# Kernel tuning notes

Measured on AMD Instinct MI355X. Metric: run time of the kernel, lower is better.

Reference implementation:

```python
import jax, jax.numpy as jnp
import numpy as np

B, SST, SL = 16, 256, 48
VOCAB, D, CH = 16384, 64, 112
TPI = 0.0


def setup_inputs() -> dict:
    key = jax.random.key(0)
    ks = jax.random.split(key, 26)
    def n(k, shp, s=0.05):
        return jax.random.normal(k, shp, dtype=jnp.float32) * s
    return {
        "x": jax.random.randint(ks[0], (B, SST), 0, VOCAB),
        "ees": n(ks[1], (B, D, SL), 1.0),
        "emb": n(ks[2], (VOCAB, D)),
        "cl0_w": n(ks[3], (CH, D, 1)),  "cl0_b": n(ks[4], (CH,)),
        "cl1_w": n(ks[5], (CH, CH, 3)), "cl1_b": n(ks[6], (CH,)),
        "claa_w": n(ks[7], (CH, CH, 3)), "claa_b": n(ks[8], (CH,)),
        "clfa_w": n(ks[9], (CH, CH, 3)), "clfa_b": n(ks[10], (CH,)),
        "ccac_w": n(ks[11], (CH, CH, 3)), "ccac_b": n(ks[12], (CH,)),
        "cib_w": n(ks[13], (D, CH, 1)),  "cib_b": n(ks[14], (D,)),
        "cpr1_w": n(ks[15], (D, 2 * D, 1)), "cpr1_b": n(ks[16], (D,)),
        "cpr2_w": n(ks[17], (D, D, 1)),  "cpr2_b": n(ks[18], (D,)),
        "cma_w": n(ks[19], (CH, D, 1)),  "cma_b": n(ks[20], (CH,)),
        "ccf_w": n(ks[21], (D, CH, 1)),  "ccf_b": n(ks[22], (D,)),
        "fff_b": n(ks[23], (VOCAB,)),
    }


def _conv1x1(x, w, b):
    # x: [B,C,S], w: [O,C,1] -> [B,O,S]
    return jnp.einsum('oc,bcs->bos', w[:, :, 0], x) + b[None, :, None]


def _conv3(x, w, b):
    # valid 1D conv, channels-first. x: [B,C,S+2] -> [B,O,S]
    y = jax.lax.conv_general_dilated(x, w, (1,), 'VALID',
                                     dimension_numbers=('NCH', 'OIH', 'NCH'))
    return y + b[None, :, None]


def _forward(x, ees, emb, cl0_w, cl0_b, cl1_w, cl1_b, claa_w, claa_b,
             clfa_w, clfa_b, ccac_w, ccac_b, cib_w, cib_b,
             cpr1_w, cpr1_b, cpr2_w, cpr2_b, cma_w, cma_b,
             ccf_w, ccf_b, fff_b):
    b = x.shape[0]
    pre_d = jnp.transpose(emb[x], (0, 2, 1))            # [B,64,SST]
    t = _conv1x1(pre_d, cl0_w, cl0_b)                   # [B,112,SST]
    tp = jnp.full((b, CH, 2), TPI, dtype=t.dtype)       # tpi pad columns

    # split cpr layer1 weight into the t-half and ees-half (concat along ch)
    wt, we = cpr1_w[:, :D, 0], cpr1_w[:, D:, 0]

    def stage(t_in, conv_w, conv_b):
        tt = jnp.concatenate([tp, t_in], axis=2)        # [B,112,SST+2]
        xconv = jax.nn.relu(_conv3(tt, conv_w, conv_b))  # [B,112,SST]
        c = _conv1x1(xconv, cib_w, cib_b)               # [B,64,SST]
        # all-pairs broadcast (sl x sst) + 1x1-conv MLP, equivalent to
        # repeat/concat/cpr in the original, without duplicating data
        h = (jnp.einsum('oc,bcs->bos', wt, c)[:, :, None, :]
             + jnp.einsum('oc,bcl->bol', we, ees)[:, :, :, None]
             + cpr1_b[None, :, None, None])             # [B,64,SL,SST]
        h = jax.nn.relu(h)
        h = jax.nn.relu(jnp.einsum('oc,bcls->bols', cpr2_w[:, :, 0], h)
                        + cpr2_b[None, :, None, None])
        m = jnp.max(h, axis=2)                          # max over sl -> [B,64,SST]
        return _conv1x1(m, cma_w, cma_b) + xconv        # residual add

    t = stage(t, cl1_w, cl1_b)
    t = stage(t, claa_w, claa_b)
    t = stage(t, clfa_w, clfa_b)
    t = stage(t, ccac_w, ccac_b)

    ccf_out = _conv1x1(t, ccf_w, ccf_b)                 # [B,64,SST]
    # tied-weight output projection: [B,SST,64] @ emb.T -> [B,SST,VOCAB]
    output = jnp.einsum('bds,vd->bsv', ccf_out, emb) + fff_b
    return output, pre_d, ccf_out


def reference(x, ees, emb, cl0_w, cl0_b, cl1_w, cl1_b, claa_w, claa_b,
              clfa_w, clfa_b, ccac_w, ccac_b, cib_w, cib_b,
              cpr1_w, cpr1_b, cpr2_w, cpr2_b, cma_w, cma_b,
              ccf_w, ccf_b, fff_b):
    return _forward(x, ees, emb, cl0_w, cl0_b, cl1_w, cl1_b, claa_w, claa_b,
                    clfa_w, clfa_b, ccac_w, ccac_b, cib_w, cib_b,
                    cpr1_w, cpr1_b, cpr2_w, cpr2_b, cma_w, cma_b,
                    ccf_w, ccf_b, fff_b)
```

## Files before the change

### kernel.cpp

```cpp
#include <hip/hip_runtime.h>

#define B_ 16
#define SST 256
#define SL 48
#define VOCAB 16384
#define D_ 64
#define CH 112

#define OUT0_ELEMS ((size_t)B_*SST*VOCAB)
#define OUT1_ELEMS (B_*D_*SST)

typedef __attribute__((ext_vector_type(8))) short s8v;
typedef __attribute__((ext_vector_type(4))) float f32x4;

#define MFMA(a,b,c) __builtin_amdgcn_mfma_f32_16x16x32_bf16(a, b, c, 0, 0, 0)

__device__ __forceinline__ void split1(float f, unsigned short* h, unsigned short* l) {
    unsigned u = __float_as_uint(f);
    *h = (unsigned short)(u >> 16);
    float lo = f - __uint_as_float(u & 0xffff0000u);
    *l = (unsigned short)(__float_as_uint(lo) >> 16);
}
__device__ __forceinline__ uint2 split_pack2(float f0, float f1) {
    unsigned u0 = __float_as_uint(f0), u1 = __float_as_uint(f1);
    unsigned hp = (u0 >> 16) | (u1 & 0xffff0000u);
    float l0 = f0 - __uint_as_float(u0 & 0xffff0000u);
    float l1 = f1 - __uint_as_float(u1 & 0xffff0000u);
    unsigned lp = (__float_as_uint(l0) >> 16) | (__float_as_uint(l1) & 0xffff0000u);
    return make_uint2(hp, lp);
}

__global__ void e_kernel(const float* __restrict__ ees,
                         const float* __restrict__ cpr1_w,
                         const float* __restrict__ cpr1_b,
                         const float* __restrict__ cib_b,
                         float* __restrict__ Eb) {
    int bl = blockIdx.x;
    int b = bl / SL, l = bl % SL;
    int tid = threadIdx.x;
    __shared__ float ec[D_];
    ec[tid] = ees[(b*D_ + tid)*SL + l];
    __syncthreads();
    const float* wrow = cpr1_w + tid*(2*D_);
    float acc = cpr1_b[tid];
    #pragma unroll
    for (int k = 0; k < D_; ++k) acc += wrow[k]*cib_b[k];
    #pragma unroll
    for (int c = 0; c < D_; ++c) acc += wrow[D_ + c]*ec[c];
    Eb[(b*SL + l)*D_ + tid] = acc;
}

__global__ void emb2bf_kernel(const float* __restrict__ emb,
                              unsigned short* __restrict__ hi,
                              unsigned short* __restrict__ lo) {
    int i = blockIdx.x*256 + threadIdx.x;
    float4 v = reinterpret_cast<const float4*>(emb)[i];
    ushort4 h, l;
    split1(v.x, &h.x, &l.x);
    split1(v.y, &h.y, &l.y);
    split1(v.z, &h.z, &l.z);
    split1(v.w, &h.w, &l.w);
    reinterpret_cast<ushort4*>(hi)[i] = h;
    reinterpret_cast<ushort4*>(lo)[i] = l;
}

__global__ void conv_prep_kernel(const float* __restrict__ w0, const float* __restrict__ w1,
                                 const float* __restrict__ w2, const float* __restrict__ w3,
                                 unsigned short* __restrict__ Wch, unsigned short* __restrict__ Wcl) {
    int gid = blockIdx.x*256 + threadIdx.x;
    int c = gid & 127;
    int o = (gid >> 7) & 127;
    int kst = gid >> 14;
    int k = kst % 3, st = kst / 3;
    const float* w = (st == 0) ? w0 : (st == 1) ? w1 : (st == 2) ? w2 : w3;
    float v = (o < CH && c < CH) ? w[o*CH*3 + c*3 + k] : 0.f;
    unsigned short h, l; split1(v, &h, &l);
    Wch[gid] = h; Wcl[gid] = l;
}

__global__ void shared_prep_kernel(const float* __restrict__ cpr1_w,
                                   const float* __restrict__ cib_w,
                                   const float* __restrict__ cpr2_w,
                                   const float* __restrict__ cma_w,
                                   const float* __restrict__ ccf_w,
                                   const float* __restrict__ cl0_w,
                                   unsigned short* __restrict__ Wcomb_h, unsigned short* __restrict__ Wcomb_l,
                                   unsigned short* __restrict__ W2h, unsigned short* __restrict__ W2l,
                                   unsigned short* __restrict__ cmah, unsigned short* __restrict__ cmal,
                                   unsigned short* __restrict__ ccfh, unsigned short* __restrict__ ccfl,
                                   unsigned short* __restrict__ cl0h, unsigned short* __restrict__ cl0l) {
    int gid = blockIdx.x*256 + threadIdx.x;
    unsigned short h, l;
    if (gid < 8192) {
        int o = gid >> 7, c = gid & 127;
        float v = 0.f;
        if (c < CH) {
            const float* wrow = cpr1_w + o*(2*D_);
            #pragma unroll
            for (int k = 0; k < D_; ++k) v += wrow[k]*cib_w[k*CH + c];
        }
        split1(v, &h, &l); Wcomb_h[gid] = h; Wcomb_l[gid] = l;
    } else if (gid < 12288) {
        int idx = gid - 8192;
        split1(cpr2_w[idx], &h, &l); W2h[idx] = h; W2l[idx] = l;
    } else if (gid < 20480) {
        int idx = gid - 12288;
        int o = idx >> 6;
        float v = (o < CH) ? cma_w[idx] : 0.f;
        split1(v, &h, &l); cmah[idx] = h; cmal[idx] = l;
    } else if (gid < 28672) {
        int idx = gid - 20480;
        int d = idx >> 7, c = idx & 127;
        float v = (c < CH) ? ccf_w[d*CH + c] : 0.f;
        split1(v, &h, &l); ccfh[idx] = h; ccfl[idx] = l;
    } else {
        int idx = gid - 28672;
        int o = idx >> 6;
        float v = (o < CH) ? cl0_w[idx] : 0.f;
        split1(v, &h, &l); cl0h[idx] = h; cl0l[idx] = l;
    }
}

__device__ __forceinline__ void h2max_wave(
    const float* __restrict__ AcRow,
    const float* __restrict__ El,
    const unsigned short* __restrict__ W2h, const unsigned short* __restrict__ W2l,
    int n, int kg, int o_lane, float b2_lane,
    unsigned short* __restrict__ Mmh, unsigned short* __restrict__ Mml, int bs) {
    float4 a00 = *reinterpret_cast<const float4*>(AcRow + kg*8);
    float4 a01 = *reinterpret_cast<const float4*>(AcRow + kg*8 + 4);
    float4 a10 = *reinterpret_cast<const float4*>(AcRow + 32 + kg*8);
    float4 a11 = *reinterpret_cast<const float4*>(AcRow + 32 + kg*8 + 4);

    f32x4 acc[4][3];
    #pragma unroll
    for (int mt = 0; mt < 4; ++mt)
        #pragma unroll
        for (int lt = 0; lt < 3; ++lt)
            acc[mt][lt] = (f32x4){0.f, 0.f, 0.f, 0.f};

    #pragma unroll
    for (int kt = 0; kt < 2; ++kt) {
        int cc = kt*32 + kg*8;
        float4 aA = (kt == 0) ? a00 : a10;
        float4 aB = (kt == 0) ? a01 : a11;
        s8v a2h[4], a2l[4];
        #pragma unroll
        for (int mt = 0; mt < 4; ++mt) {
            a2h[mt] = *(const s8v*)&W2h[(mt*16 + n)*64 + cc];
            a2l[mt] = *(const s8v*)&W2l[(mt*16 + n)*64 + cc];
        }
        #pragma unroll
        for (int lt = 0; lt < 3; ++lt) {
            const float* ep = &El[(lt*16 + n)*68 + cc];
            float4 e0 = *reinterpret_cast<const float4*>(ep);
            float4 e1 = *reinterpret_cast<const float4*>(ep + 4);
            float h0 = fmaxf(aA.x + e0.x, 0.f);
            float h1 = fmaxf(aA.y + e0.y, 0.f);
            float h2 = fmaxf(aA.z + e0.z, 0.f);
            float h3 = fmaxf(aA.w + e0.w, 0.f);
            float h4 = fmaxf(aB.x + e1.x, 0.f);
            float h5 = fmaxf(aB.y + e1.y, 0.f);
            float h6 = fmaxf(aB.z + e1.z, 0.f);
            float h7 = fmaxf(aB.w + e1.w, 0.f);
            uint2 q0 = split_pack2(h0, h1);
            uint2 q1 = split_pack2(h2, h3);
            uint2 q2 = split_pack2(h4, h5);
            uint2 q3 = split_pack2(h6, h7);
            union { unsigned u[4]; s8v v; } Bh, Bl;
            Bh.u[0] = q0.x; Bh.u[1] = q1.x; Bh.u[2] = q2.x; Bh.u[3] = q3.x;
            Bl.u[0] = q0.y; Bl.u[1] = q1.y; Bl.u[2] = q2.y; Bl.u[3] = q3.y;
            #pragma unroll
            for (int mt = 0; mt < 4; ++mt) {
                acc[mt][lt] = MFMA(a2h[mt], Bh.v, acc[mt][lt]);
                acc[mt][lt] = MFMA(a2h[mt], Bl.v, acc[mt][lt]);
                acc[mt][lt] = MFMA(a2l[mt], Bh.v, acc[mt][lt]);
            }
        }
    }

    float mx[16];
    #pragma unroll
    for (int mt = 0; mt < 4; ++mt)
        #pragma unroll
        for (int r = 0; r < 4; ++r)
            mx[mt*4 + r] = fmaxf(fmaxf(acc[mt][0][r], acc[mt][1][r]), acc[mt][2][r]);
    #pragma unroll
    for (int step = 0; step < 4; ++step) {
        int msk = 1 << step;
        #pragma unroll
        for (int i = 0; i < 16; ++i)
            mx[i] = fmaxf(mx[i], __shfl_xor(mx[i], msk));
    }
    float sel = mx[0];
    #pragma unroll
    for (int i = 1; i < 16; ++i)
        sel = (n == i) ? mx[i] : sel;
    float mval = fmaxf(sel + b2_lane, 0.f);
    unsigned short mh, ml; split1(mval, &mh, &ml);
    Mmh[bs*64 + o_lane] = mh;
    Mml[bs*64 + o_lane] = ml;
}

__global__ __launch_bounds__(512) void stage1_kernel(
    const int* __restrict__ x, const float* __restrict__ emb,
    const unsigned short* __restrict__ cl0h, const unsigned short* __restrict__ cl0l,
    const float* __restrict__ cl0_b,
    const unsigned short* __restrict__ Wch, const unsigned short* __restrict__ Wcl,
    const float* __restrict__ conv_b,
    const unsigned short* __restrict__ Wcombh, const unsigned short* __restrict__ Wcombl,
    const float* __restrict__ Eb,
    const unsigned short* __restrict__ W2h, const unsigned short* __restrict__ W2l,
    const float* __restrict__ cpr2_b,
    float* __restrict__ pre_d, float* __restrict__ xc_g,
    unsigned short* __restrict__ Mmh, unsigned short* __restrict__ Mml) {
    int b = blockIdx.x >> 4, s0 = (blockIdx.x & 15) << 4;
    int tid = threadIdx.x, w = tid >> 6, lane = tid & 63, n = lane & 15, kg = lane >> 4;

    __shared__ unsigned short Eg_h[18*72], Eg_l[18*72];
    __shared__ unsigned short Tt_h[18*136], Tt_l[18*136];
    __shared__ unsigned short Xt_h[16*136], Xt_l[16*136];
    __shared__ float El[48*68];
    __shared__ float AcT[16*68];

    for (int idx = tid; idx < 288; idx += 512) {
        int si = idx >> 4, c4 = (idx & 15)*4;
        int s = s0 - 2 + si;
        float4 v = make_float4(0.f, 0.f, 0.f, 0.f);
        if (s >= 0) {
            int tok = x[b*SST + s];
            v = *reinterpret_cast<const float4*>(&emb[tok*D_ + c4]);
        }
        ushort4 h, l;
        split1(v.x, &h.x, &l.x); split1(v.y, &h.y, &l.y);
        split1(v.z, &h.z, &l.z); split1(v.w, &h.w, &l.w);
        *reinterpret_cast<ushort4*>(&Eg_h[si*72 + c4]) = h;
        *reinterpret_cast<ushort4*>(&Eg_l[si*72 + c4]) = l;
        if (si >= 2) {
            pre_d[(b*D_ + c4+0)*SST + s] = v.x;
            pre_d[(b*D_ + c4+1)*SST + s] = v.y;
            pre_d[(b*D_ + c4+2)*SST + s] = v.z;
            pre_d[(b*D_ + c4+3)*SST + s] = v.w;
        }
    }
    for (int idx = tid; idx < 768; idx += 512) {
        int l = idx >> 4, c4 = (idx & 15)*4;
        *reinterpret_cast<float4*>(&El[l*68 + c4]) =
            *reinterpret_cast<const float4*>(&Eb[(b*SL + l)*64 + c4]);
    }
    __syncthreads();

    int ob = w*16 + kg*4;
    #pragma unroll
    for (int ct = 0; ct < 2; ++ct) {
        int si = ct*2 + n;
        f32x4 tv = {0.f, 0.f, 0.f, 0.f};
        #pragma unroll
        for (int kt = 0; kt < 2; ++kt) {
            int cc = kt*32 + kg*8;
            s8v bh = *(const s8v*)&Eg_h[si*72 + cc];
            s8v bl = *(const s8v*)&Eg_l[si*72 + cc];
            int ai = (w*16 + n)*64 + cc;
            s8v ah = *(const s8v*)&cl0h[ai];
            s8v al = *(const s8v*)&cl0l[ai];
            tv = MFMA(ah, bh, tv); tv = MFMA(ah, bl, tv); tv = MFMA(al, bh, tv);
        }
        int s = s0 - 2 + si;
        float r0 = 0.f, r1 = 0.f, r2 = 0.f, r3 = 0.f;
        if (s >= 0) {
            r0 = tv[0] + ((ob+0 < CH) ? cl0_b[ob+0] : 0.f);
            r1 = tv[1] + ((ob+1 < CH) ? cl0_b[ob+1] : 0.f);
            r2 = tv[2] + ((ob+2 < CH) ? cl0_b[ob+2] : 0.f);
            r3 = tv[3] + ((ob+3 < CH) ? cl0_b[ob+3] : 0.f);
        }
        uint2 p01 = split_pack2(r0, r1), p23 = split_pack2(r2, r3);
        *reinterpret_cast<uint2*>(&Tt_h[si*136 + ob]) = make_uint2(p01.x, p23.x);
        *reinterpret_cast<uint2*>(&Tt_l[si*136 + ob]) = make_uint2(p01.y, p23.y);
    }
    __syncthreads();

    f32x4 xcv = {0.f, 0.f, 0.f, 0.f};
    #pragma unroll
    for (int k = 0; k < 3; ++k)
        #pragma unroll
        for (int kt = 0; kt < 4; ++kt) {
            int cc = kt*32 + kg*8;
            s8v bh = *(const s8v*)&Tt_h[(n + k)*136 + cc];
            s8v bl = *(const s8v*)&Tt_l[(n + k)*136 + cc];
            int ai = (k*128 + w*16 + n)*128 + cc;
            s8v ah = *(const s8v*)&Wch[ai];
            s8v al = *(const s8v*)&Wcl[ai];
            xcv = MFMA(ah, bh, xcv); xcv = MFMA(ah, bl, xcv); xcv = MFMA(al, bh, xcv);
        }
    #pragma unroll
    for (int r = 0; r < 4; ++r) {
        float cb = (ob + r < CH) ? conv_b[ob + r] : 0.f;
        xcv[r] = fmaxf(xcv[r] + cb, 0.f);
    }
    {
        uint2 p01 = split_pack2(xcv[0], xcv[1]), p23 = split_pack2(xcv[2], xcv[3]);
        *reinterpret_cast<uint2*>(&Xt_h[n*136 + ob]) = make_uint2(p01.x, p23.x);
        *reinterpret_cast<uint2*>(&Xt_l[n*136 + ob]) = make_uint2(p01.y, p23.y);
        *reinterpret_cast<float4*>(&xc_g[(b*SST + s0 + n)*128 + ob]) =
            make_float4(xcv[0], xcv[1], xcv[2], xcv[3]);
    }
    __syncthreads();

    if (w < 4) {
        f32x4 acc = {0.f, 0.f, 0.f, 0.f};
        #pragma unroll
        for (int kt = 0; kt < 4; ++kt) {
            int cc = kt*32 + kg*8;
            int ai = (w*16 + n)*128 + cc;
            s8v ah = *(const s8v*)&Wcombh[ai];
            s8v al = *(const s8v*)&Wcombl[ai];
            s8v bh = *(const s8v*)&Xt_h[n*136 + cc];
            s8v bl = *(const s8v*)&Xt_l[n*136 + cc];
            acc = MFMA(ah, bh, acc); acc = MFMA(ah, bl, acc); acc = MFMA(al, bh, acc);
        }
        *reinterpret_cast<float4*>(&AcT[n*68 + w*16 + kg*4]) =
            make_float4(acc[0], acc[1], acc[2], acc[3]);
    }
    __syncthreads();

    int o_lane = ((n >> 2) << 4) + (kg << 2) + (n & 3);
    float b2_lane = cpr2_b[o_lane];
    #pragma unroll
    for (int si = 0; si < 2; ++si) {
        int s = w*2 + si;
        h2max_wave(&AcT[s*68], El, W2h, W2l, n, kg, o_lane, b2_lane,
                   Mmh, Mml, b*SST + s0 + s);
    }
}

__global__ __launch_bounds__(512) void stagem_kernel(
    const unsigned short* __restrict__ Mmh_in, const unsigned short* __restrict__ Mml_in,
    const unsigned short* __restrict__ cmah, const unsigned short* __restrict__ cmal,
    const float* __restrict__ cma_b, const float* __restrict__ xc_prev,
    const unsigned short* __restrict__ Wch, const unsigned short* __restrict__ Wcl,
    const float* __restrict__ conv_b,
    const unsigned short* __restrict__ Wcombh, const unsigned short* __restrict__ Wcombl,
    const float* __restrict__ Eb,
    const unsigned short* __restrict__ W2h, const unsigned short* __restrict__ W2l,
    const float* __restrict__ cpr2_b,
    float* __restrict__ xc_g,
    unsigned short* __restrict__ Mmh_out, unsigned short* __restrict__ Mml_out) {
    int b = blockIdx.x >> 4, s0 = (blockIdx.x & 15) << 4;
    int tid = threadIdx.x, w = tid >> 6, lane = tid & 63, n = lane & 15, kg = lane >> 4;

    __shared__ unsigned short Eg_h[18*72], Eg_l[18*72];
    __shared__ unsigned short Tt_h[18*136], Tt_l[18*136];
    __shared__ unsigned short Xt_h[16*136], Xt_l[16*136];
    __shared__ float El[48*68];
    __shared__ float AcT[16*68];

    for (int idx = tid; idx < 288; idx += 512) {
        int si = idx >> 4, c4 = (idx & 15)*4;
        int s = s0 - 2 + si;
        uint2 h = make_uint2(0, 0), l = make_uint2(0, 0);
        if (s >= 0) {
            h = *reinterpret_cast<const uint2*>(&Mmh_in[(b*SST + s)*64 + c4]);
            l = *reinterpret_cast<const uint2*>(&Mml_in[(b*SST + s)*64 + c4]);
        }
        *reinterpret_cast<uint2*>(&Eg_h[si*72 + c4]) = h;
        *reinterpret_cast<uint2*>(&Eg_l[si*72 + c4]) = l;
    }
    for (int idx = tid; idx < 768; idx += 512) {
        int l = idx >> 4, c4 = (idx & 15)*4;
        *reinterpret_cast<float4*>(&El[l*68 + c4]) =
            *reinterpret_cast<const float4*>(&Eb[(b*SL + l)*64 + c4]);
    }
    __syncthreads();

    int ob = w*16 + kg*4;
    #pragma unroll
    for (int ct = 0; ct < 2; ++ct) {
        int si = ct*2 + n;
        f32x4 tv = {0.f, 0.f, 0.f, 0.f};
        #pragma unroll
        for (int kt = 0; kt < 2; ++kt) {
            int cc = kt*32 + kg*8;
            s8v bh = *(const s8v*)&Eg_h[si*72 + cc];
            s8v bl = *(const s8v*)&Eg_l[si*72 + cc];
            int ai = (w*16 + n)*64 + cc;
            s8v ah = *(const s8v*)&cmah[ai];
            s8v al = *(const s8v*)&cmal[ai];
            tv = MFMA(ah, bh, tv); tv = MFMA(ah, bl, tv); tv = MFMA(al, bh, tv);
        }
        int s = s0 - 2 + si;
        float r0 = 0.f, r1 = 0.f, r2 = 0.f, r3 = 0.f;
        if (s >= 0) {
            float4 xr = *reinterpret_cast<const float4*>(&xc_prev[(b*SST + s)*128 + ob]);
            r0 = tv[0] + ((ob+0 < CH) ? cma_b[ob+0] : 0.f) + xr.x;
            r1 = tv[1] + ((ob+1 < CH) ? cma_b[ob+1] : 0.f) + xr.y;
            r2 = tv[2] + ((ob+2 < CH) ? cma_b[ob+2] : 0.f) + xr.z;
            r3 = tv[3] + ((ob+3 < CH) ? cma_b[ob+3] : 0.f) + xr.w;
        }
        uint2 p01 = split_pack2(r0, r1), p23 = split_pack2(r2, r3);
        *reinterpret_cast<uint2*>(&Tt_h[si*136 + ob]) = make_uint2(p01.x, p23.x);
        *reinterpret_cast<uint2*>(&Tt_l[si*136 + ob]) = make_uint2(p01.y, p23.y);
    }
    __syncthreads();

    f32x4 xcv = {0.f, 0.f, 0.f, 0.f};
    #pragma unroll
    for (int k = 0; k < 3; ++k)
        #pragma unroll
        for (int kt = 0; kt < 4; ++kt) {
            int cc = kt*32 + kg*8;
            s8v bh = *(const s8v*)&Tt_h[(n + k)*136 + cc];
            s8v bl = *(const s8v*)&Tt_l[(n + k)*136 + cc];
            int ai = (k*128 + w*16 + n)*128 + cc;
            s8v ah = *(const s8v*)&Wch[ai];
            s8v al = *(const s8v*)&Wcl[ai];
            xcv = MFMA(ah, bh, xcv); xcv = MFMA(ah, bl, xcv); xcv = MFMA(al, bh, xcv);
        }
    #pragma unroll
    for (int r = 0; r < 4; ++r) {
        float cb = (ob + r < CH) ? conv_b[ob + r] : 0.f;
        xcv[r] = fmaxf(xcv[r] + cb, 0.f);
    }
    {
        uint2 p01 = split_pack2(xcv[0], xcv[1]), p23 = split_pack2(xcv[2], xcv[3]);
        *reinterpret_cast<uint2*>(&Xt_h[n*136 + ob]) = make_uint2(p01.x, p23.x);
        *reinterpret_cast<uint2*>(&Xt_l[n*136 + ob]) = make_uint2(p01.y, p23.y);
        *reinterpret_cast<float4*>(&xc_g[(b*SST + s0 + n)*128 + ob]) =
            make_float4(xcv[0], xcv[1], xcv[2], xcv[3]);
    }
    __syncthreads();

    if (w < 4) {
        f32x4 acc = {0.f, 0.f, 0.f, 0.f};
        #pragma unroll
        for (int kt = 0; kt < 4; ++kt) {
            int cc = kt*32 + kg*8;
            int ai = (w*16 + n)*128 + cc;
            s8v ah = *(const s8v*)&Wcombh[ai];
            s8v al = *(const s8v*)&Wcombl[ai];
            s8v bh = *(const s8v*)&Xt_h[n*136 + cc];
            s8v bl = *(const s8v*)&Xt_l[n*136 + cc];
            acc = MFMA(ah, bh, acc); acc = MFMA(ah, bl, acc); acc = MFMA(al, bh, acc);
        }
        *reinterpret_cast<float4*>(&AcT[n*68 + w*16 + kg*4]) =
            make_float4(acc[0], acc[1], acc[2], acc[3]);
    }
    __syncthreads();

    int o_lane = ((n >> 2) << 4) + (kg << 2) + (n & 3);
    float b2_lane = cpr2_b[o_lane];
    #pragma unroll
    for (int si = 0; si < 2; ++si) {
        int s = w*2 + si;
        h2max_wave(&AcT[s*68], El, W2h, W2l, n, kg, o_lane, b2_lane,
                   Mmh_out, Mml_out, b*SST + s0 + s);
    }
}

__global__ __launch_bounds__(256) void cmaccf_kernel(
    const unsigned short* __restrict__ Mmh, const unsigned short* __restrict__ Mml,
    const unsigned short* __restrict__ cmah, const unsigned short* __restrict__ cmal,
    const float* __restrict__ cma_b, const float* __restrict__ xc_prev,
    const unsigned short* __restrict__ ccfh, const unsigned short* __restrict__ ccfl,
    const float* __restrict__ ccf_b,
    float* __restrict__ ccf_out,
    unsigned short* __restrict__ Ahi, unsigned short* __restrict__ Alo) {
    int b = blockIdx.x >> 4, s0 = (blockIdx.x & 15) << 4;
    int tid = threadIdx.x, w = tid >> 6, lane = tid & 63, n = lane & 15, kg = lane >> 4;

    __shared__ unsigned short Mh[16*72], Ml[16*72];
    __shared__ unsigned short Th[16*136], Tl[16*136];

    for (int idx = tid; idx < 256; idx += 256) {
        int s = idx >> 4, c4 = (idx & 15)*4;
        *reinterpret_cast<uint2*>(&Mh[s*72 + c4]) =
            *reinterpret_cast<const uint2*>(&Mmh[(b*SST + s0 + s)*64 + c4]);
        *reinterpret_cast<uint2*>(&Ml[s*72 + c4]) =
            *reinterpret_cast<const uint2*>(&Mml[(b*SST + s0 + s)*64 + c4]);
    }
    __syncthreads();

    #pragma unroll
    for (int half = 0; half < 2; ++half) {
        int ob = (half*4 + w)*16 + kg*4;
        f32x4 tv = {0.f, 0.f, 0.f, 0.f};
        #pragma unroll
        for (int kt = 0; kt < 2; ++kt) {
            int cc = kt*32 + kg*8;
            s8v bh = *(const s8v*)&Mh[n*72 + cc];
            s8v bl = *(const s8v*)&Ml[n*72 + cc];
            int ai = ((half*4 + w)*16 + n)*64 + cc;
            s8v ah = *(const s8v*)&cmah[ai];
            s8v al = *(const s8v*)&cmal[ai];
            tv = MFMA(ah, bh, tv); tv = MFMA(ah, bl, tv); tv = MFMA(al, bh, tv);
        }
        int s = s0 + n;
        float4 xr = *reinterpret_cast<const float4*>(&xc_prev[(b*SST + s)*128 + ob]);
        float r0 = tv[0] + ((ob+0 < CH) ? cma_b[ob+0] : 0.f) + xr.x;
        float r1 = tv[1] + ((ob+1 < CH) ? cma_b[ob+1] : 0.f) + xr.y;
        float r2 = tv[2] + ((ob+2 < CH) ? cma_b[ob+2] : 0.f) + xr.z;
        float r3 = tv[3] + ((ob+3 < CH) ? cma_b[ob+3] : 0.f) + xr.w;
        uint2 p01 = split_pack2(r0, r1), p23 = split_pack2(r2, r3);
        *reinterpret_cast<uint2*>(&Th[n*136 + ob]) = make_uint2(p01.x, p23.x);
        *reinterpret_cast<uint2*>(&Tl[n*136 + ob]) = make_uint2(p01.y, p23.y);
    }
    __syncthreads();

    f32x4 acc = {0.f, 0.f, 0.f, 0.f};
    #pragma unroll
    for (int kt = 0; kt < 4; ++kt) {
        int cc = kt*32 + kg*8;
        int ai = (w*16 + n)*128 + cc;
        s8v ah = *(const s8v*)&ccfh[ai];
        s8v al = *(const s8v*)&ccfl[ai];
        s8v bh = *(const s8v*)&Th[n*136 + cc];
        s8v bl = *(const s8v*)&Tl[n*136 + cc];
        acc = MFMA(ah, bh, acc); acc = MFMA(ah, bl, acc); acc = MFMA(al, bh, acc);
    }
    int d0 = w*16 + kg*4, s = s0 + n;
    float v0 = acc[0] + ccf_b[d0+0];
    float v1 = acc[1] + ccf_b[d0+1];
    float v2 = acc[2] + ccf_b[d0+2];
    float v3 = acc[3] + ccf_b[d0+3];
    ccf_out[(b*D_ + d0+0)*SST + s] = v0;
    ccf_out[(b*D_ + d0+1)*SST + s] = v1;
    ccf_out[(b*D_ + d0+2)*SST + s] = v2;
    ccf_out[(b*D_ + d0+3)*SST + s] = v3;
    uint2 p01 = split_pack2(v0, v1), p23 = split_pack2(v2, v3);
    *reinterpret_cast<uint2*>(&Ahi[(b*SST + s)*64 + d0]) = make_uint2(p01.x, p23.x);
    *reinterpret_cast<uint2*>(&Alo[(b*SST + s)*64 + d0]) = make_uint2(p01.y, p23.y);
}

__global__ __launch_bounds__(256) void logits_mfma_kernel(
    const unsigned short* __restrict__ Ahi,
    const unsigned short* __restrict__ Alo,
    const unsigned short* __restrict__ Bhi,
    const unsigned short* __restrict__ Blo,
    const float* __restrict__ fffb,
    float* __restrict__ out) {
    int ntile = blockIdx.x & 127;
    int mtile = blockIdx.x >> 7;
    int wid = threadIdx.x >> 6;
    int lane = threadIdx.x & 63;
    int wm = wid >> 1, wn = wid & 1;
    int m0 = mtile*128 + wm*64;
    int v0 = ntile*128 + wn*64;
    int row16 = lane & 15, kg = lane >> 4;

    const short* Ah = (const short*)Ahi;
    const short* Al = (const short*)Alo;
    const short* Bh = (const short*)Bhi;
    const short* Bl = (const short*)Blo;

    f32x4 acc[4][4];
    #pragma unroll
    for (int mi = 0; mi < 4; ++mi)
        #pragma unroll
        for (int ni = 0; ni < 4; ++ni)
            acc[mi][ni] = (f32x4){0.f, 0.f, 0.f, 0.f};

    #pragma unroll
    for (int kk = 0; kk < 2; ++kk) {
        int koff = kk*32 + kg*8;
        s8v ah[4], al[4], bh[4], bl[4];
        #pragma unroll
        for (int mi = 0; mi < 4; ++mi) {
            int r = (m0 + mi*16 + row16)*D_ + koff;
            ah[mi] = *reinterpret_cast<const s8v*>(Ah + r);
            al[mi] = *reinterpret_cast<const s8v*>(Al + r);
        }
        #pragma unroll
        for (int ni = 0; ni < 4; ++ni) {
            int r = (v0 + ni*16 + row16)*D_ + koff;
            bh[ni] = *reinterpret_cast<const s8v*>(Bh + r);
            bl[ni] = *reinterpret_cast<const s8v*>(Bl + r);
        }
        #pragma unroll
        for (int mi = 0; mi < 4; ++mi)
            #pragma unroll
            for (int ni = 0; ni < 4; ++ni) {
                acc[mi][ni] = MFMA(ah[mi], bh[ni], acc[mi][ni]);
                acc[mi][ni] = MFMA(ah[mi], bl[ni], acc[mi][ni]);
                acc[mi][ni] = MFMA(al[mi], bh[ni], acc[mi][ni]);
            }
    }

    float fb[4];
    #pragma unroll
    for (int ni = 0; ni < 4; ++ni) fb[ni] = fffb[v0 + ni*16 + row16];

    #pragma unroll
    for (int mi = 0; mi < 4; ++mi) {
        #pragma unroll
        for (int r = 0; r < 4; ++r) {
            size_t rowbase = (size_t)(m0 + mi*16 + kg*4 + r)*VOCAB;
            #pragma unroll
            for (int ni = 0; ni < 4; ++ni) {
                out[rowbase + v0 + ni*16 + row16] = acc[mi][ni][r] + fb[ni];
            }
        }
    }
}

extern "C" void kernel_launch(void* const* d_in, const int* in_sizes, int n_in,
                              void* d_out, int out_size, void* d_ws, size_t ws_size,
                              hipStream_t stream) {
    const int*   x     = (const int*)d_in[0];
    const float* ees   = (const float*)d_in[1];
    const float* emb   = (const float*)d_in[2];
    const float* cl0_w = (const float*)d_in[3];
    const float* cl0_b = (const float*)d_in[4];
    const float* cl1_w = (const float*)d_in[5];
    const float* cl1_b = (const float*)d_in[6];
    const float* claa_w= (const float*)d_in[7];
    const float* claa_b= (const float*)d_in[8];
    const float* clfa_w= (const float*)d_in[9];
    const float* clfa_b= (const float*)d_in[10];
    const float* ccac_w= (const float*)d_in[11];
    const float* ccac_b= (const float*)d_in[12];
    const float* cib_w = (const float*)d_in[13];
    const float* cib_b = (const float*)d_in[14];
    const float* cpr1_w= (const float*)d_in[15];
    const float* cpr1_b= (const float*)d_in[16];
    const float* cpr2_w= (const float*)d_in[17];
    const float* cpr2_b= (const float*)d_in[18];
    const float* cma_w = (const float*)d_in[19];
    const float* cma_b = (const float*)d_in[20];
    const float* ccf_w = (const float*)d_in[21];
    const float* ccf_b = (const float*)d_in[22];
    const float* fff_b = (const float*)d_in[23];

    float* out = (float*)d_out;
    float* out_pre = out + OUT0_ELEMS;
    float* out_ccf = out_pre + OUT1_ELEMS;

    unsigned short* EmbHi = (unsigned short*)d_ws;
    unsigned short* EmbLo = EmbHi + VOCAB*D_;
    unsigned short* Ahi   = EmbLo + VOCAB*D_;
    unsigned short* Alo   = Ahi + B_*SST*D_;

    char* sc = (char*)d_out + (size_t)16*1024*1024;
    float*          Eb    = (float*)sc;            sc += B_*SL*D_*4;
    unsigned short* Wch   = (unsigned short*)sc;   sc += 4*3*128*128*2;
    unsigned short* Wcl   = (unsigned short*)sc;   sc += 4*3*128*128*2;
    unsigned short* Wcombh= (unsigned short*)sc;   sc += 64*128*2;
    unsigned short* Wcombl= (unsigned short*)sc;   sc += 64*128*2;
    unsigned short* W2h   = (unsigned short*)sc;   sc += 64*64*2;
    unsigned short* W2l   = (unsigned short*)sc;   sc += 64*64*2;
    unsigned short* cmah  = (unsigned short*)sc;   sc += 128*64*2;
    unsigned short* cmal  = (unsigned short*)sc;   sc += 128*64*2;
    unsigned short* ccfh  = (unsigned short*)sc;   sc += 64*128*2;
    unsigned short* ccfl  = (unsigned short*)sc;   sc += 64*128*2;
    unsigned short* cl0h  = (unsigned short*)sc;   sc += 128*64*2;
    unsigned short* cl0l  = (unsigned short*)sc;   sc += 128*64*2;
    float*          xc_a  = (float*)sc;            sc += (size_t)B_*SST*128*4;
    float*          xc_b  = (float*)sc;            sc += (size_t)B_*SST*128*4;
    unsigned short* Mmh   = (unsigned short*)sc;   sc += B_*SST*64*2;
    unsigned short* Mml   = (unsigned short*)sc;   sc += B_*SST*64*2;

    conv_prep_kernel<<<768, 256, 0, stream>>>(cl1_w, claa_w, clfa_w, ccac_w, Wch, Wcl);
    shared_prep_kernel<<<144, 256, 0, stream>>>(cpr1_w, cib_w, cpr2_w, cma_w, ccf_w, cl0_w,
        Wcombh, Wcombl, W2h, W2l, cmah, cmal, ccfh, ccfl, cl0h, cl0l);
    emb2bf_kernel<<<VOCAB*D_/4/256, 256, 0, stream>>>(emb, EmbHi, EmbLo);
    e_kernel<<<B_*SL, 64, 0, stream>>>(ees, cpr1_w, cpr1_b, cib_b, Eb);

    const int WCS = 3*128*128;
    stage1_kernel<<<256, 512, 0, stream>>>(x, emb, cl0h, cl0l, cl0_b,
        Wch + 0*WCS, Wcl + 0*WCS, cl1_b, Wcombh, Wcombl, Eb, W2h, W2l, cpr2_b,
        out_pre, xc_a, Mmh, Mml);
    stagem_kernel<<<256, 512, 0, stream>>>(Mmh, Mml, cmah, cmal, cma_b, xc_a,
        Wch + 1*WCS, Wcl + 1*WCS, claa_b, Wcombh, Wcombl, Eb, W2h, W2l, cpr2_b,
        xc_b, Mmh, Mml);
    stagem_kernel<<<256, 512, 0, stream>>>(Mmh, Mml, cmah, cmal, cma_b, xc_b,
        Wch + 2*WCS, Wcl + 2*WCS, clfa_b, Wcombh, Wcombl, Eb, W2h, W2l, cpr2_b,
        xc_a, Mmh, Mml);
    stagem_kernel<<<256, 512, 0, stream>>>(Mmh, Mml, cmah, cmal, cma_b, xc_a,
        Wch + 3*WCS, Wcl + 3*WCS, ccac_b, Wcombh, Wcombl, Eb, W2h, W2l, cpr2_b,
        xc_b, Mmh, Mml);

    cmaccf_kernel<<<256, 256, 0, stream>>>(Mmh, Mml, cmah, cmal, cma_b, xc_b,
        ccfh, ccfl, ccf_b, out_ccf, Ahi, Alo);
    logits_mfma_kernel<<<(B_*SST/128)*(VOCAB/128), 256, 0, stream>>>(
        Ahi, Alo, EmbHi, EmbLo, fff_b, out);
}
```

Before: 170.3 us.

## Fuse four stage kernels into one cooperative kernel with grid syncs

Replaces the four separate stage kernel launches with a single cooperative persistent kernel that loops over stages and uses grid.sync between them. M buffers are double-buffered, because one block reads neighboring sequence rows written by other blocks. The aim is to remove launch gaps and reload only the Eb tile once per block. It risks grid-sync overhead, and cooperative launch limits on residency with 512-thread blocks and large shared memory use.

Result: slower. 271.1 us (+59.2%).

```diff
diff --git a/kernel.cpp b/kernel.cpp
--- a/kernel.cpp
+++ b/kernel.cpp
@@ -1,4 +1,7 @@
 #include <hip/hip_runtime.h>
+#include <hip/hip_cooperative_groups.h>
+
+namespace cg = cooperative_groups;
 
 #define B_ 16
 #define SST 256
@@ -6,6 +9,7 @@
 #define VOCAB 16384
 #define D_ 64
 #define CH 112
+#define WCS (3*128*128)
 
 #define OUT0_ELEMS ((size_t)B_*SST*VOCAB)
 #define OUT1_ELEMS (B_*D_*SST)
@@ -202,18 +206,22 @@
     Mml[bs*64 + o_lane] = ml;
 }
 
-__global__ __launch_bounds__(512) void stage1_kernel(
-    const int* __restrict__ x, const float* __restrict__ emb,
-    const unsigned short* __restrict__ cl0h, const unsigned short* __restrict__ cl0l,
-    const float* __restrict__ cl0_b,
-    const unsigned short* __restrict__ Wch, const unsigned short* __restrict__ Wcl,
-    const float* __restrict__ conv_b,
-    const unsigned short* __restrict__ Wcombh, const unsigned short* __restrict__ Wcombl,
-    const float* __restrict__ Eb,
-    const unsigned short* __restrict__ W2h, const unsigned short* __restrict__ W2l,
-    const float* __restrict__ cpr2_b,
-    float* __restrict__ pre_d, float* __restrict__ xc_g,
-    unsigned short* __restrict__ Mmh, unsigned short* __restrict__ Mml) {
+struct SArgs {
+    const int* x; const float* emb;
+    const unsigned short *cl0h, *cl0l; const float* cl0_b;
+    const unsigned short *Wch, *Wcl;
+    const float *cb0, *cb1, *cb2, *cb3;
+    const unsigned short *cmah, *cmal; const float* cma_b;
+    const unsigned short *Wcombh, *Wcombl;
+    const float* Eb;
+    const unsigned short *W2h, *W2l; const float* cpr2_b;
+    float* pre_d;
+    float *xc_a, *xc_b;
+    unsigned short *MmhA, *MmlA, *MmhB, *MmlB;
+};
+
+__global__ __launch_bounds__(512) void stages_kernel(SArgs a) {
+    cg::grid_group grid = cg::this_grid();
     int b = blockIdx.x >> 4, s0 = (blockIdx.x & 15) << 4;
     int tid = threadIdx.x, w = tid >> 6, lane = tid & 63, n = lane & 15, kg = lane >> 4;
 
@@ -223,236 +231,155 @@
     __shared__ float El[48*68];
     __shared__ float AcT[16*68];
 
-    for (int idx = tid; idx < 288; idx += 512) {
-        int si = idx >> 4, c4 = (idx & 15)*4;
-        int s = s0 - 2 + si;
-        float4 v = make_float4(0.f, 0.f, 0.f, 0.f);
-        if (s >= 0) {
-            int tok = x[b*SST + s];
-            v = *reinterpret_cast<const float4*>(&emb[tok*D_ + c4]);
-        }
-        ushort4 h, l;
-        split1(v.x, &h.x, &l.x); split1(v.y, &h.y, &l.y);
-        split1(v.z, &h.z, &l.z); split1(v.w, &h.w, &l.w);
-        *reinterpret_cast<ushort4*>(&Eg_h[si*72 + c4]) = h;
-        *reinterpret_cast<ushort4*>(&Eg_l[si*72 + c4]) = l;
-        if (si >= 2) {
-            pre_d[(b*D_ + c4+0)*SST + s] = v.x;
-            pre_d[(b*D_ + c4+1)*SST + s] = v.y;
-            pre_d[(b*D_ + c4+2)*SST + s] = v.z;
-            pre_d[(b*D_ + c4+3)*SST + s] = v.w;
-        }
-    }
     for (int idx = tid; idx < 768; idx += 512) {
         int l = idx >> 4, c4 = (idx & 15)*4;
         *reinterpret_cast<float4*>(&El[l*68 + c4]) =
-            *reinterpret_cast<const float4*>(&Eb[(b*SL + l)*64 + c4]);
-    }
-    __syncthreads();
+            *reinterpret_cast<const float4*>(&a.Eb[(b*SL + l)*64 + c4]);
+    }
 
     int ob = w*16 + kg*4;
-    #pragma unroll
-    for (int ct = 0; ct < 2; ++ct) {
-        int si = ct*2 + n;
-        f32x4 tv = {0.f, 0.f, 0.f, 0.f};
-        #pragma unroll
-        for (int kt = 0; kt < 2; ++kt) {
-            int cc = kt*32 + kg*8;
-            s8v bh = *(const s8v*)&Eg_h[si*72 + cc];
-            s8v bl = *(const s8v*)&Eg_l[si*72 + cc];
-            int ai = (w*16 + n)*64 + cc;
-            s8v ah = *(const s8v*)&cl0h[ai];
-            s8v al = *(const s8v*)&cl0l[ai];
-            tv = MFMA(ah, bh, tv); tv = MFMA(ah, bl, tv); tv = MFMA(al, bh, tv);
-        }
-        int s = s0 - 2 + si;
-        float r0 = 0.f, r1 = 0.f, r2 = 0.f, r3 = 0.f;
-        if (s >= 0) {
-            r0 = tv[0] + ((ob+0 < CH) ? cl0_b[ob+0] : 0.f);
-            r1 = tv[1] + ((ob+1 < CH) ? cl0_b[ob+1] : 0.f);
-            r2 = tv[2] + ((ob+2 < CH) ? cl0_b[ob+2] : 0.f);
-            r3 = tv[3] + ((ob+3 < CH) ? cl0_b[ob+3] : 0.f);
-        }
-        uint2 p01 = split_pack2(r0, r1), p23 = split_pack2(r2, r3);
-        *reinterpret_cast<uint2*>(&Tt_h[si*136 + ob]) = make_uint2(p01.x, p23.x);
-        *reinterpret_cast<uint2*>(&Tt_l[si*136 + ob]) = make_uint2(p01.y, p23.y);
-    }
-    __syncthreads();
-
-    f32x4 xcv = {0.f, 0.f, 0.f, 0.f};
-    #pragma unroll
-    for (int k = 0; k < 3; ++k)
-        #pragma unroll
-        for (int kt = 0; kt < 4; ++kt) {
-            int cc = kt*32 + kg*8;
-            s8v bh = *(const s8v*)&Tt_h[(n + k)*136 + cc];
-            s8v bl = *(const s8v*)&Tt_l[(n + k)*136 + cc];
-            int ai = (k*128 + w*16 + n)*128 + cc;
-            s8v ah = *(const s8v*)&Wch[ai];
-            s8v al = *(const s8v*)&Wcl[ai];
-            xcv = MFMA(ah, bh, xcv); xcv = MFMA(ah, bl, xcv); xcv = MFMA(al, bh, xcv);
-        }
-    #pragma unroll
-    for (int r = 0; r < 4; ++r) {
-        float cb = (ob + r < CH) ? conv_b[ob + r] : 0.f;
-        xcv[r] = fmaxf(xcv[r] + cb, 0.f);
-    }
-    {
-        uint2 p01 = split_pack2(xcv[0], xcv[1]), p23 = split_pack2(xcv[2], xcv[3]);
-        *reinterpret_cast<uint2*>(&Xt_h[n*136 + ob]) = make_uint2(p01.x, p23.x);
-        *reinterpret_cast<uint2*>(&Xt_l[n*136 + ob]) = make_uint2(p01.y, p23.y);
-        *reinterpret_cast<float4*>(&xc_g[(b*SST + s0 + n)*128 + ob]) =
-            make_float4(xcv[0], xcv[1], xcv[2], xcv[3]);
-    }
-    __syncthreads();
-
-    if (w < 4) {
-        f32x4 acc = {0.f, 0.f, 0.f, 0.f};
-        #pragma unroll
-        for (int kt = 0; kt < 4; ++kt) {
-            int cc = kt*32 + kg*8;
-            int ai = (w*16 + n)*128 + cc;
-            s8v ah = *(const s8v*)&Wcombh[ai];
-            s8v al = *(const s8v*)&Wcombl[ai];
-            s8v bh = *(const s8v*)&Xt_h[n*136 + cc];
-            s8v bl = *(const s8v*)&Xt_l[n*136 + cc];
-            acc = MFMA(ah, bh, acc); acc = MFMA(ah, bl, acc); acc = MFMA(al, bh, acc);
-        }
-        *reinterpret_cast<float4*>(&AcT[n*68 + w*16 + kg*4]) =
-            make_float4(acc[0], acc[1], acc[2], acc[3]);
-    }
-    __syncthreads();
-
     int o_lane = ((n >> 2) << 4) + (kg << 2) + (n & 3);
-    float b2_lane = cpr2_b[o_lane];
-    #pragma unroll
-    for (int si = 0; si < 2; ++si) {
-        int s = w*2 + si;
-        h2max_wave(&AcT[s*68], El, W2h, W2l, n, kg, o_lane, b2_lane,
-                   Mmh, Mml, b*SST + s0 + s);
-    }
-}
-
-__global__ __launch_bounds__(512) void stagem_kernel(
-    const unsigned short* __restrict__ Mmh_in, const unsigned short* __restrict__ Mml_in,
-    const unsigned short* __restrict__ cmah, const unsigned short* __restrict__ cmal,
-    const float* __restrict__ cma_b, const float* __restrict__ xc_prev,
-    const unsigned short* __restrict__ Wch, const unsigned short* __restrict__ Wcl,
-    const float* __restrict__ conv_b,
-    const unsigned short* __restrict__ Wcombh, const unsigned short* __restrict__ Wcombl,
-    const float* __restrict__ Eb,
-    const unsigned short* __restrict__ W2h, const unsigned short* __restrict__ W2l,
-    const float* __restrict__ cpr2_b,
-    float* __restrict__ xc_g,
-    unsigned short* __restrict__ Mmh_out, unsigned short* __restrict__ Mml_out) {
-    int b = blockIdx.x >> 4, s0 = (blockIdx.x & 15) << 4;
-    int tid = threadIdx.x, w = tid >> 6, lane = tid & 63, n = lane & 15, kg = lane >> 4;
-
-    __shared__ unsigned short Eg_h[18*72], Eg_l[18*72];
-    __shared__ unsigned short Tt_h[18*136], Tt_l[18*136];
-    __shared__ unsigned short Xt_h[16*136], Xt_l[16*136];
-    __shared__ float El[48*68];
-    __shared__ float AcT[16*68];
-
-    for (int idx = tid; idx < 288; idx += 512) {
-        int si = idx >> 4, c4 = (idx & 15)*4;
-        int s = s0 - 2 + si;
-        uint2 h = make_uint2(0, 0), l = make_uint2(0, 0);
-        if (s >= 0) {
-            h = *reinterpret_cast<const uint2*>(&Mmh_in[(b*SST + s)*64 + c4]);
-            l = *reinterpret_cast<const uint2*>(&Mml_in[(b*SST + s)*64 + c4]);
-        }
-        *reinterpret_cast<uint2*>(&Eg_h[si*72 + c4]) = h;
-        *reinterpret_cast<uint2*>(&Eg_l[si*72 + c4]) = l;
-    }
-    for (int idx = tid; idx < 768; idx += 512) {
-        int l = idx >> 4, c4 = (idx & 15)*4;
-        *reinterpret_cast<float4*>(&El[l*68 + c4]) =
-            *reinterpret_cast<const float4*>(&Eb[(b*SL + l)*64 + c4]);
-    }
-    __syncthreads();
-
-    int ob = w*16 + kg*4;
-    #pragma unroll
-    for (int ct = 0; ct < 2; ++ct) {
-        int si = ct*2 + n;
-        f32x4 tv = {0.f, 0.f, 0.f, 0.f};
-        #pragma unroll
-        for (int kt = 0; kt < 2; ++kt) {
-            int cc = kt*32 + kg*8;
-            s8v bh = *(const s8v*)&Eg_h[si*72 + cc];
-            s8v bl = *(const s8v*)&Eg_l[si*72 + cc];
-            int ai = (w*16 + n)*64 + cc;
-            s8v ah = *(const s8v*)&cmah[ai];
-            s8v al = *(const s8v*)&cmal[ai];
-            tv = MFMA(ah, bh, tv); tv = MFMA(ah, bl, tv); tv = MFMA(al, bh, tv);
-        }
-        int s = s0 - 2 + si;
-        float r0 = 0.f, r1 = 0.f, r2 = 0.f, r3 = 0.f;
-        if (s >= 0) {
-            float4 xr = *reinterpret_cast<const float4*>(&xc_prev[(b*SST + s)*128 + ob]);
-            r0 = tv[0] + ((ob+0 < CH) ? cma_b[ob+0] : 0.f) + xr.x;
-            r1 = tv[1] + ((ob+1 < CH) ? cma_b[ob+1] : 0.f) + xr.y;
-            r2 = tv[2] + ((ob+2 < CH) ? cma_b[ob+2] : 0.f) + xr.z;
-            r3 = tv[3] + ((ob+3 < CH) ? cma_b[ob+3] : 0.f) + xr.w;
-        }
-        uint2 p01 = split_pack2(r0, r1), p23 = split_pack2(r2, r3);
-        *reinterpret_cast<uint2*>(&Tt_h[si*136 + ob]) = make_uint2(p01.x, p23.x);
-        *reinterpret_cast<uint2*>(&Tt_l[si*136 + ob]) = make_uint2(p01.y, p23.y);
-    }
-    __syncthreads();
-
-    f32x4 xcv = {0.f, 0.f, 0.f, 0.f};
-    #pragma unroll
-    for (int k = 0; k < 3; ++k)
-        #pragma unroll
-        for (int kt = 0; kt < 4; ++kt) {
-            int cc = kt*32 + kg*8;
-            s8v bh = *(const s8v*)&Tt_h[(n + k)*136 + cc];
-            s8v bl = *(const s8v*)&Tt_l[(n + k)*136 + cc];
-            int ai = (k*128 + w*16 + n)*128 + cc;
-            s8v ah = *(const s8v*)&Wch[ai];
-            s8v al = *(const s8v*)&Wcl[ai];
-            xcv = MFMA(ah, bh, xcv); xcv = MFMA(ah, bl, xcv); xcv = MFMA(al, bh, xcv);
-        }
-    #pragma unroll
-    for (int r = 0; r < 4; ++r) {
-        float cb = (ob + r < CH) ? conv_b[ob + r] : 0.f;
-        xcv[r] = fmaxf(xcv[r] + cb, 0.f);
-    }
-    {
-        uint2 p01 = split_pack2(xcv[0], xcv[1]), p23 = split_pack2(xcv[2], xcv[3]);
-        *reinterpret_cast<uint2*>(&Xt_h[n*136 + ob]) = make_uint2(p01.x, p23.x);
-        *reinterpret_cast<uint2*>(&Xt_l[n*136 + ob]) = make_uint2(p01.y, p23.y);
-        *reinterpret_cast<float4*>(&xc_g[(b*SST + s0 + n)*128 + ob]) =
-            make_float4(xcv[0], xcv[1], xcv[2], xcv[3]);
-    }
-    __syncthreads();
-
-    if (w < 4) {
-        f32x4 acc = {0.f, 0.f, 0.f, 0.f};
-        #pragma unroll
-        for (int kt = 0; kt < 4; ++kt) {
-            int cc = kt*32 + kg*8;
-            int ai = (w*16 + n)*128 + cc;
-            s8v ah = *(const s8v*)&Wcombh[ai];
-            s8v al = *(const s8v*)&Wcombl[ai];
-            s8v bh = *(const s8v*)&Xt_h[n*136 + cc];
-            s8v bl = *(const s8v*)&Xt_l[n*136 + cc];
-            acc = MFMA(ah, bh, acc); acc = MFMA(ah, bl, acc); acc = MFMA(al, bh, acc);
-        }
-        *reinterpret_cast<float4*>(&AcT[n*68 + w*16 + kg*4]) =
-            make_float4(acc[0], acc[1], acc[2], acc[3]);
-    }
-    __syncthreads();
-
-    int o_lane = ((n >> 2) << 4) + (kg << 2) + (n & 3);
-    float b2_lane = cpr2_b[o_lane];
-    #pragma unroll
-    for (int si = 0; si < 2; ++si) {
-        int s = w*2 + si;
-        h2max_wave(&AcT[s*68], El, W2h, W2l, n, kg, o_lane, b2_lane,
-                   Mmh_out, Mml_out, b*SST + s0 + s);
+    float b2_lane = a.cpr2_b[o_lane];
+    const int tbase = b*SST;
+
+    for (int st = 0; st < 4; ++st) {
+        const unsigned short* Wc_h = a.Wch + st*WCS;
+        const unsigned short* Wc_l = a.Wcl + st*WCS;
+        const float* conv_b = (st == 0) ? a.cb0 : (st == 1) ? a.cb1 : (st == 2) ? a.cb2 : a.cb3;
+        const unsigned short* Mi_h = (st & 1) ? a.MmhA : a.MmhB;
+        const unsigned short* Mi_l = (st & 1) ? a.MmlA : a.MmlB;
+        unsigned short* Mo_h = (st & 1) ? a.MmhB : a.MmhA;
+        unsigned short* Mo_l = (st & 1) ? a.MmlB : a.MmlA;
+        const float* xc_prev = (st & 1) ? a.xc_a : a.xc_b;
+        float* xc_out = (st & 1) ? a.xc_b : a.xc_a;
+
+        if (st == 0) {
+            for (int idx = tid; idx < 288; idx += 512) {
+                int si = idx >> 4, c4 = (idx & 15)*4;
+                int s = s0 - 2 + si;
+                float4 v = make_float4(0.f, 0.f, 0.f, 0.f);
+                if (s >= 0) {
+                    int tok = a.x[tbase + s];
+                    v = *reinterpret_cast<const float4*>(&a.emb[tok*D_ + c4]);
+                }
+                ushort4 h, l;
+                split1(v.x, &h.x, &l.x); split1(v.y, &h.y, &l.y);
+                split1(v.z, &h.z, &l.z); split1(v.w, &h.w, &l.w);
+                *reinterpret_cast<ushort4*>(&Eg_h[si*72 + c4]) = h;
+                *reinterpret_cast<ushort4*>(&Eg_l[si*72 + c4]) = l;
+                if (si >= 2) {
+                    a.pre_d[(b*D_ + c4+0)*SST + s] = v.x;
+                    a.pre_d[(b*D_ + c4+1)*SST + s] = v.y;
+                    a.pre_d[(b*D_ + c4+2)*SST + s] = v.z;
+                    a.pre_d[(b*D_ + c4+3)*SST + s] = v.w;
+                }
+            }
+        } else {
+            for (int idx = tid; idx < 288; idx += 512) {
+                int si = idx >> 4, c4 = (idx & 15)*4;
+                int s = s0 - 2 + si;
+                uint2 h = make_uint2(0, 0), l = make_uint2(0, 0);
+                if (s >= 0) {
+                    h = *reinterpret_cast<const uint2*>(&Mi_h[(tbase + s)*64 + c4]);
+                    l = *reinterpret_cast<const uint2*>(&Mi_l[(tbase + s)*64 + c4]);
+                }
+                *reinterpret_cast<uint2*>(&Eg_h[si*72 + c4]) = h;
+                *reinterpret_cast<uint2*>(&Eg_l[si*72 + c4]) = l;
+            }
+        }
+        __syncthreads();
+
+        #pragma unroll
+        for (int ct = 0; ct < 2; ++ct) {
+            int si = ct*2 + n;
+            f32x4 tv = {0.f, 0.f, 0.f, 0.f};
+            #pragma unroll
+            for (int kt = 0; kt < 2; ++kt) {
+                int cc = kt*32 + kg*8;
+                s8v bh = *(const s8v*)&Eg_h[si*72 + cc];
+                s8v bl = *(const s8v*)&Eg_l[si*72 + cc];
+                int ai = (w*16 + n)*64 + cc;
+                s8v ah, al;
+                if (st == 0) {
+                    ah = *(const s8v*)&a.cl0h[ai];
+                    al = *(const s8v*)&a.cl0l[ai];
+                } else {
+                    ah = *(const s8v*)&a.cmah[ai];
+                    al = *(const s8v*)&a.cmal[ai];
+                }
+                tv = MFMA(ah, bh, tv); tv = MFMA(ah, bl, tv); tv = MFMA(al, bh, tv);
+            }
+            int s = s0 - 2 + si;
+            float r0 = 0.f, r1 = 0.f, r2 = 0.f, r3 = 0.f;
+            if (s >= 0) {
+                const float* hb = (st == 0) ? a.cl0_b : a.cma_b;
+                r0 = tv[0] + ((ob+0 < CH) ? hb[ob+0] : 0.f);
+                r1 = tv[1] + ((ob+1 < CH) ? hb[ob+1] : 0.f);
+                r2 = tv[2] + ((ob+2 < CH) ? hb[ob+2] : 0.f);
+                r3 = tv[3] + ((ob+3 < CH) ? hb[ob+3] : 0.f);
+                if (st != 0) {
+                    float4 xr = *reinterpret_cast<const float4*>(&xc_prev[(tbase + s)*128 + ob]);
+                    r0 += xr.x; r1 += xr.y; r2 += xr.z; r3 += xr.w;
+                }
+            }
+            uint2 p01 = split_pack2(r0, r1), p23 = split_pack2(r2, r3);
+            *reinterpret_cast<uint2*>(&Tt_h[si*136 + ob]) = make_uint2(p01.x, p23.x);
+            *reinterpret_cast<uint2*>(&Tt_l[si*136 + ob]) = make_uint2(p01.y, p23.y);
+        }
+        __syncthreads();
+
+        f32x4 xcv = {0.f, 0.f, 0.f, 0.f};
+        #pragma unroll
+        for (int k = 0; k < 3; ++k)
+            #pragma unroll
+            for (int kt = 0; kt < 4; ++kt) {
+                int cc = kt*32 + kg*8;
+                s8v bh = *(const s8v*)&Tt_h[(n + k)*136 + cc];
+                s8v bl = *(const s8v*)&Tt_l[(n + k)*136 + cc];
+                int ai = (k*128 + w*16 + n)*128 + cc;
+                s8v ah = *(const s8v*)&Wc_h[ai];
+                s8v al = *(const s8v*)&Wc_l[ai];
+                xcv = MFMA(ah, bh, xcv); xcv = MFMA(ah, bl, xcv); xcv = MFMA(al, bh, xcv);
+            }
+        #pragma unroll
+        for (int r = 0; r < 4; ++r) {
+            float cb = (ob + r < CH) ? conv_b[ob + r] : 0.f;
+            xcv[r] = fmaxf(xcv[r] + cb, 0.f);
+        }
+        {
+            uint2 p01 = split_pack2(xcv[0], xcv[1]), p23 = split_pack2(xcv[2], xcv[3]);
+            *reinterpret_cast<uint2*>(&Xt_h[n*136 + ob]) = make_uint2(p01.x, p23.x);
+            *reinterpret_cast<uint2*>(&Xt_l[n*136 + ob]) = make_uint2(p01.y, p23.y);
+            *reinterpret_cast<float4*>(&xc_out[(tbase + s0 + n)*128 + ob]) =
+                make_float4(xcv[0], xcv[1], xcv[2], xcv[3]);
+        }
+        __syncthreads();
+
+        if (w < 4) {
+            f32x4 acc = {0.f, 0.f, 0.f, 0.f};
+            #pragma unroll
+            for (int kt = 0; kt < 4; ++kt) {
+                int cc = kt*32 + kg*8;
+                int ai = (w*16 + n)*128 + cc;
+                s8v ah = *(const s8v*)&a.Wcombh[ai];
+                s8v al = *(const s8v*)&a.Wcombl[ai];
+                s8v bh = *(const s8v*)&Xt_h[n*136 + cc];
+                s8v bl = *(const s8v*)&Xt_l[n*136 + cc];
+                acc = MFMA(ah, bh, acc); acc = MFMA(ah, bl, acc); acc = MFMA(al, bh, acc);
+            }
+            *reinterpret_cast<float4*>(&AcT[n*68 + w*16 + kg*4]) =
+                make_float4(acc[0], acc[1], acc[2], acc[3]);
+        }
+        __syncthreads();
+
+        #pragma unroll
+        for (int si = 0; si < 2; ++si) {
+            int s = w*2 + si;
+            h2max_wave(&AcT[s*68], El, a.W2h, a.W2l, n, kg, o_lane, b2_lane,
+                       Mo_h, Mo_l, tbase + s0 + s);
+        }
+
+        if (st < 3) grid.sync();
     }
 }
 
@@ -654,8 +581,10 @@
     unsigned short* cl0l  = (unsigned short*)sc;   sc += 128*64*2;
     float*          xc_a  = (float*)sc;            sc += (size_t)B_*SST*128*4;
     float*          xc_b  = (float*)sc;            sc += (size_t)B_*SST*128*4;
-    unsigned short* Mmh   = (unsigned short*)sc;   sc += B_*SST*64*2;
-    unsigned short* Mml   = (unsigned short*)sc;   sc += B_*SST*64*2;
+    unsigned short* MmhA  = (unsigned short*)sc;   sc += B_*SST*64*2;
+    unsigned short* MmlA  = (unsigned short*)sc;   sc += B_*SST*64*2;
+    unsigned short* MmhB  = (unsigned short*)sc;   sc += B_*SST*64*2;
+    unsigned short* MmlB  = (unsigned short*)sc;   sc += B_*SST*64*2;
 
     conv_prep_kernel<<<768, 256, 0, stream>>>(cl1_w, claa_w, clfa_w, ccac_w, Wch, Wcl);
     shared_prep_kernel<<<144, 256, 0, stream>>>(cpr1_w, cib_w, cpr2_w, cma_w, ccf_w, cl0_w,
@@ -663,21 +592,22 @@
     emb2bf_kernel<<<VOCAB*D_/4/256, 256, 0, stream>>>(emb, EmbHi, EmbLo);
     e_kernel<<<B_*SL, 64, 0, stream>>>(ees, cpr1_w, cpr1_b, cib_b, Eb);
 
-    const int WCS = 3*128*128;
-    stage1_kernel<<<256, 512, 0, stream>>>(x, emb, cl0h, cl0l, cl0_b,
-        Wch + 0*WCS, Wcl + 0*WCS, cl1_b, Wcombh, Wcombl, Eb, W2h, W2l, cpr2_b,
-        out_pre, xc_a, Mmh, Mml);
-    stagem_kernel<<<256, 512, 0, stream>>>(Mmh, Mml, cmah, cmal, cma_b, xc_a,
-        Wch + 1*WCS, Wcl + 1*WCS, claa_b, Wcombh, Wcombl, Eb, W2h, W2l, cpr2_b,
-        xc_b, Mmh, Mml);
-    stagem_kernel<<<256, 512, 0, stream>>>(Mmh, Mml, cmah, cmal, cma_b, xc_b,
-        Wch + 2*WCS, Wcl + 2*WCS, clfa_b, Wcombh, Wcombl, Eb, W2h, W2l, cpr2_b,
-        xc_a, Mmh, Mml);
-    stagem_kernel<<<256, 512, 0, stream>>>(Mmh, Mml, cmah, cmal, cma_b, xc_a,
-        Wch + 3*WCS, Wcl + 3*WCS, ccac_b, Wcombh, Wcombl, Eb, W2h, W2l, cpr2_b,
-        xc_b, Mmh, Mml);
-
-    cmaccf_kernel<<<256, 256, 0, stream>>>(Mmh, Mml, cmah, cmal, cma_b, xc_b,
+    SArgs sa;
+    sa.x = x; sa.emb = emb;
+    sa.cl0h = cl0h; sa.cl0l = cl0l; sa.cl0_b = cl0_b;
+    sa.Wch = Wch; sa.Wcl = Wcl;
+    sa.cb0 = cl1_b; sa.cb1 = claa_b; sa.cb2 = clfa_b; sa.cb3 = ccac_b;
+    sa.cmah = cmah; sa.cmal = cmal; sa.cma_b = cma_b;
+    sa.Wcombh = Wcombh; sa.Wcombl = Wcombl;
+    sa.Eb = Eb;
+    sa.W2h = W2h; sa.W2l = W2l; sa.cpr2_b = cpr2_b;
+    sa.pre_d = out_pre;
+    sa.xc_a = xc_a; sa.xc_b = xc_b;
+    sa.MmhA = MmhA; sa.MmlA = MmlA; sa.MmhB = MmhB; sa.MmlB = MmlB;
+    void* kargs[] = { &sa };
+    hipLaunchCooperativeKernel(stages_kernel, dim3(256), dim3(512), kargs, 0, stream);
+
+    cmaccf_kernel<<<256, 256, 0, stream>>>(MmhB, MmlB, cmah, cmal, cma_b, xc_b,
         ccfh, ccfl, ccf_b, out_ccf, Ahi, Alo);
     logits_mfma_kernel<<<(B_*SST/128)*(VOCAB/128), 256, 0, stream>>>(
         Ahi, Alo, EmbHi, EmbLo, fff_b, out);
```
